# Kernel optimization log

Measured on AMD Instinct MI355X. Metric: run time of the kernel, lower is better.

Reference implementation:

```python
import jax, jax.numpy as jnp
import numpy as np
import math

D_MODEL = 1024
NUM_HEADS = 16
D_KEY = D_MODEL // NUM_HEADS  # 64, used only for the softmax scale
B, S = 4, 2048


def setup_inputs() -> dict:
    key = jax.random.key(0)
    ks = jax.random.split(key, 7)
    scale = 1.0 / math.sqrt(D_MODEL)
    x = jax.random.normal(ks[0], (B, S, D_MODEL), dtype=jnp.float32)
    # torch.nn.Linear params: weight [out, in], bias [out]
    Wq = jax.random.normal(ks[1], (D_MODEL, D_MODEL), dtype=jnp.float32) * scale
    bq = jax.random.normal(ks[2], (D_MODEL,), dtype=jnp.float32) * scale
    Wk = jax.random.normal(ks[3], (D_MODEL, D_MODEL), dtype=jnp.float32) * scale
    bk = jax.random.normal(ks[4], (D_MODEL,), dtype=jnp.float32) * scale
    Wv = jax.random.normal(ks[5], (D_MODEL, D_MODEL), dtype=jnp.float32) * scale
    bv = jax.random.normal(ks[6], (D_MODEL,), dtype=jnp.float32) * scale
    return {"x": x, "Wq": Wq, "bq": bq, "Wk": Wk, "bk": bk, "Wv": Wv, "bv": bv}


def reference(x, Wq, bq, Wk, bk, Wv, bv):
    # Q, K, V projections (torch Linear: x @ W.T + b)
    Q = jnp.einsum('bsd,ed->bse', x, Wq) + bq  # [B,S,D]
    K = jnp.einsum('bsd,ed->bse', x, Wk) + bk
    V = jnp.einsum('bsd,ed->bse', x, Wv) + bv
    inv_sqrt_dk = 1.0 / math.sqrt(D_KEY)
    # full-width attention (no head split, as in the source forward)
    scores = jnp.einsum('bqd,bkd->bqk', Q, K) * inv_sqrt_dk  # [B,S,S]
    weights = jax.nn.softmax(scores, axis=-1)
    return jnp.einsum('bqk,bkd->bqd', weights, V)  # [B,S,D]
```

## Files before the change

kernel.cpp:

```cpp
#include <hip/hip_runtime.h>
#include <stdint.h>

#define S_LEN 2048
#define DMODEL 1024
#define NBATCH 4
#define MROWS (NBATCH * S_LEN)

typedef __bf16 bf16x8 __attribute__((ext_vector_type(8)));
typedef float f32x4 __attribute__((ext_vector_type(4)));

__device__ __forceinline__ unsigned short f2bf(float f) {
  unsigned int x = __builtin_bit_cast(unsigned int, f);
  x += 0x7FFFu + ((x >> 16) & 1u);
  return (unsigned short)(x >> 16);
}

template <int N>
__device__ __forceinline__ void waitvm() {
  static_assert(N <= 8, "vmcnt range");
  if constexpr (N < 0) {}
  else if constexpr (N == 0) asm volatile("s_waitcnt vmcnt(0)" ::: "memory");
  else if constexpr (N == 1) asm volatile("s_waitcnt vmcnt(1)" ::: "memory");
  else if constexpr (N == 2) asm volatile("s_waitcnt vmcnt(2)" ::: "memory");
  else if constexpr (N == 3) asm volatile("s_waitcnt vmcnt(3)" ::: "memory");
  else if constexpr (N == 4) asm volatile("s_waitcnt vmcnt(4)" ::: "memory");
  else if constexpr (N == 5) asm volatile("s_waitcnt vmcnt(5)" ::: "memory");
  else if constexpr (N == 6) asm volatile("s_waitcnt vmcnt(6)" ::: "memory");
  else if constexpr (N == 7) asm volatile("s_waitcnt vmcnt(7)" ::: "memory");
  else asm volatile("s_waitcnt vmcnt(8)" ::: "memory");
}
#define BARRIER() do { __builtin_amdgcn_s_barrier(); asm volatile("" ::: "memory"); } while (0)

__global__ void cvt_kernel(const float* __restrict__ src, ushort4* __restrict__ dst, int n4) {
  int i = blockIdx.x * blockDim.x + threadIdx.x;
  if (i < n4) {
    float4 v = reinterpret_cast<const float4*>(src)[i];
    ushort4 o;
    o.x = f2bf(v.x); o.y = f2bf(v.y); o.z = f2bf(v.z); o.w = f2bf(v.w);
    dst[i] = o;
  }
}

template <int BM_, int EP>
__global__ __launch_bounds__(512, 2) void gemm8(
    const unsigned short* __restrict__ A, const unsigned short* __restrict__ Bm,
    void* __restrict__ Cp, const float* __restrict__ bias,
    int lda, int ldb, int ldc, int NT, float scale,
    long zsA, long zsB, long zsC) {
  constexpr int BN_ = 256;
  constexpr int BK = 64;
  constexpr int RA = BM_ / 128;
  constexpr int HALF_A = (BM_ / 2) * 128;
  constexpr int HALF_B = 128 * 128;
  constexpr int ATILE = BM_ * 128;
  constexpr int BTILE = BN_ * 128;
  constexpr int MREP = BM_ / 32;
  constexpr int MQ = MREP / 2;
  constexpr int VPRO = (BM_ == 256) ? 4 : 3;
  constexpr int V_P0 = (BM_ == 256) ? 4 : 2;
  constexpr int V_P3 = (BM_ == 256) ? 8 : 6;
  constexpr int V_P5 = (BM_ == 256) ? 4 : 3;
  constexpr int VD_P0 = (BM_ == 256) ? 2 : 1;

  __shared__ alignas(16) char lds[(ATILE + BTILE) * 2];

  const int tid = threadIdx.x;
  const int l = tid & 63;
  const int w = tid >> 6;
  const int wm = w >> 2;
  const int wn = w & 3;

  const int gx = gridDim.x;
  const int nwg = gridDim.x * gridDim.y;
  int n = blockIdx.y * gx + blockIdx.x;
  int n2 = (n & 7) * (nwg >> 3) + (n >> 3);
  const int tileM = (n2 / gx) * BM_;
  const int tileN = (n2 % gx) * BN_;

  const int z = blockIdx.z;
  const unsigned short* Ab = A + (size_t)z * zsA;
  const unsigned short* Bb = Bm + (size_t)z * zsB;

  const int srow = l >> 3;
  const int scol = (((l & 7) ^ srow) * 16);

  auto stageA = [&](int buf, int t, int h) {
#pragma unroll
    for (int r = 0; r < RA; ++r) {
      int row = h * (BM_ / 2) + r * 64 + w * 8 + srow;
      const char* g = (const char*)(Ab + (size_t)(tileM + row) * lda + t * BK) + scol;
      char* d = lds + buf * (ATILE + BTILE) + h * HALF_A + r * 8192 + w * 1024;
      __builtin_amdgcn_global_load_lds(
          (const __attribute__((address_space(1))) void*)g,
          (__attribute__((address_space(3))) void*)d, 16, 0, 0);
    }
  };
  auto stageB = [&](int buf, int t, int h) {
#pragma unroll
    for (int r = 0; r < 2; ++r) {
      int row = h * 128 + r * 64 + w * 8 + srow;
      const char* g = (const char*)(Bb + (size_t)(tileN + row) * ldb + t * BK) + scol;
      char* d = lds + buf * (ATILE + BTILE) + ATILE + h * HALF_B + r * 8192 + w * 1024;
      __builtin_amdgcn_global_load_lds(
          (const __attribute__((address_space(1))) void*)g,
          (__attribute__((address_space(3))) void*)d, 16, 0, 0);
    }
  };

  f32x4 acc[MREP][4];
#pragma unroll
  for (int m = 0; m < MREP; ++m)
#pragma unroll
    for (int nn = 0; nn < 4; ++nn) acc[m][nn] = f32x4{0.f, 0.f, 0.f, 0.f};

  const int frow = l & 15;
  auto rdA = [&](int buf, int mh, int m, int kk) -> bf16x8 {
    int row = mh * (BM_ / 2) + wm * (BM_ / 4) + m * 16 + frow;
    int col = (kk * 64 + ((l >> 4) * 16)) ^ ((row & 7) << 4);
    return *reinterpret_cast<const bf16x8*>(lds + buf * (ATILE + BTILE) + row * 128 + col);
  };
  auto rdB = [&](int buf, int nh, int nn, int kk) -> bf16x8 {
    int row = nh * 128 + wn * 32 + nn * 16 + frow;
    int col = (kk * 64 + ((l >> 4) * 16)) ^ ((row & 7) << 4);
    return *reinterpret_cast<const bf16x8*>(lds + buf * (ATILE + BTILE) + ATILE + row * 128 + col);
  };

  bf16x8 avA[MQ], avB[MQ];
  bf16x8 bvv[2][2][2];

  auto rdAset = [&](int buf, int mh, int kk, bf16x8 (&dst)[MQ]) {
#pragma unroll
    for (int m = 0; m < MQ; ++m) dst[m] = rdA(buf, mh, m, kk);
  };
  auto rdBset = [&](int buf, int nh, int kk) {
#pragma unroll
    for (int nn = 0; nn < 2; ++nn) bvv[nh][kk][nn] = rdB(buf, nh, nn, kk);
  };
  auto mf8 = [&](bf16x8 (&av)[MQ], int mh, int nh, int kk) {
    __builtin_amdgcn_s_setprio(1);
#pragma unroll
    for (int m = 0; m < MQ; ++m)
#pragma unroll
      for (int nn = 0; nn < 2; ++nn)
        acc[mh * MQ + m][nh * 2 + nn] = __builtin_amdgcn_mfma_f32_16x16x32_bf16(
            av[m], bvv[nh][kk][nn], acc[mh * MQ + m][nh * 2 + nn], 0, 0, 0);
    __builtin_amdgcn_s_setprio(0);
  };

  stageA(0, 0, 0);
  stageB(0, 0, 0);
  stageB(0, 0, 1);
  stageA(0, 0, 1);
  waitvm<VPRO>();
  BARRIER();

  for (int t = 0; t < NT - 1; ++t) {
    const int buf = t & 1, nb = buf ^ 1;
    rdAset(buf, 0, 0, avA); rdBset(buf, 0, 0);
    stageA(nb, t + 1, 0); waitvm<V_P0>(); BARRIER();
    mf8(avA, 0, 0, 0);
    rdBset(buf, 1, 0);
    stageB(nb, t + 1, 0); BARRIER();
    mf8(avA, 0, 1, 0);
    rdAset(buf, 0, 1, avB); rdBset(buf, 1, 1);
    stageB(nb, t + 1, 1); BARRIER();
    mf8(avB, 0, 1, 1);
    rdBset(buf, 0, 1);
    stageA(nb, t + 1, 1); waitvm<V_P3>(); BARRIER();
    mf8(avB, 0, 0, 1);
    rdAset(buf, 1, 1, avA);
    BARRIER();
    mf8(avA, 1, 0, 1); mf8(avA, 1, 1, 1);
    rdAset(buf, 1, 0, avB);
    waitvm<V_P5>(); BARRIER();
    mf8(avB, 1, 1, 0); mf8(avB, 1, 0, 0);
  }
  {
    const int buf = (NT - 1) & 1;
    rdAset(buf, 0, 0, avA); rdBset(buf, 0, 0); waitvm<VD_P0>(); BARRIER();
    mf8(avA, 0, 0, 0);
    rdBset(buf, 1, 0); BARRIER();
    mf8(avA, 0, 1, 0);
    rdAset(buf, 0, 1, avB); rdBset(buf, 1, 1); BARRIER();
    mf8(avB, 0, 1, 1);
    rdBset(buf, 0, 1); waitvm<0>(); BARRIER();
    mf8(avB, 0, 0, 1);
    rdAset(buf, 1, 1, avA); BARRIER();
    mf8(avA, 1, 0, 1); mf8(avA, 1, 1, 1);
    rdAset(buf, 1, 0, avB); BARRIER();
    mf8(avB, 1, 1, 0); mf8(avB, 1, 0, 0);
  }

  const int lr = (l >> 4) * 4;
  const int lc = l & 15;
#pragma unroll
  for (int mh = 0; mh < 2; ++mh) {
#pragma unroll
    for (int m = 0; m < MQ; ++m) {
#pragma unroll
      for (int nh = 0; nh < 2; ++nh) {
#pragma unroll
        for (int nn = 0; nn < 2; ++nn) {
          int gr = tileM + mh * (BM_ / 2) + wm * (BM_ / 4) + m * 16 + lr;
          int gc = tileN + nh * 128 + wn * 32 + nn * 16 + lc;
          f32x4 v = acc[mh * MQ + m][nh * 2 + nn];
          if constexpr (EP == 0 || EP == 3) {
            unsigned short* C = (unsigned short*)Cp + (size_t)z * zsC;
#pragma unroll
            for (int j = 0; j < 4; ++j) {
              float bb = (EP == 0) ? bias[gc] : bias[gr + j];
              C[(size_t)(gr + j) * ldc + gc] = f2bf(v[j] + bb);
            }
          } else {
            float* C = (float*)Cp + (size_t)z * zsC;
#pragma unroll
            for (int j = 0; j < 4; ++j)
              C[(size_t)(gr + j) * ldc + gc] = (EP == 1) ? v[j] * scale : v[j];
          }
        }
      }
    }
  }
}

__global__ __launch_bounds__(256) void softmax_kernel(const float* __restrict__ Sb,
                                                      unsigned short* __restrict__ P) {
  const size_t row = blockIdx.x;
  const float* sp = Sb + row * S_LEN;
  const int t = threadIdx.x;
  const int wid = t >> 6, lane = t & 63;
  float4 v0 = reinterpret_cast<const float4*>(sp)[t * 2];
  float4 v1 = reinterpret_cast<const float4*>(sp)[t * 2 + 1];
  float s[8] = {v0.x, v0.y, v0.z, v0.w, v1.x, v1.y, v1.z, v1.w};
  float mx = s[0];
#pragma unroll
  for (int i = 1; i < 8; ++i) mx = fmaxf(mx, s[i]);
#pragma unroll
  for (int o = 32; o > 0; o >>= 1) mx = fmaxf(mx, __shfl_xor(mx, o));
  __shared__ float redm[4];
  __shared__ float reds[4];
  if (lane == 0) redm[wid] = mx;
  __syncthreads();
  mx = fmaxf(fmaxf(redm[0], redm[1]), fmaxf(redm[2], redm[3]));
  float e[8];
  float sum = 0.f;
#pragma unroll
  for (int i = 0; i < 8; ++i) { e[i] = __expf(s[i] - mx); sum += e[i]; }
#pragma unroll
  for (int o = 32; o > 0; o >>= 1) sum += __shfl_xor(sum, o);
  if (lane == 0) reds[wid] = sum;
  __syncthreads();
  sum = reds[0] + reds[1] + reds[2] + reds[3];
  float inv = 1.0f / sum;
  ushort4 o0, o1;
  o0.x = f2bf(e[0] * inv); o0.y = f2bf(e[1] * inv); o0.z = f2bf(e[2] * inv); o0.w = f2bf(e[3] * inv);
  o1.x = f2bf(e[4] * inv); o1.y = f2bf(e[5] * inv); o1.z = f2bf(e[6] * inv); o1.w = f2bf(e[7] * inv);
  ushort4* dp = reinterpret_cast<ushort4*>(P + row * S_LEN);
  dp[t * 2] = o0;
  dp[t * 2 + 1] = o1;
}

extern "C" void kernel_launch(void* const* d_in, const int* in_sizes, int n_in,
                              void* d_out, int out_size, void* d_ws, size_t ws_size,
                              hipStream_t stream) {
  (void)in_sizes; (void)n_in; (void)out_size;
  const float* x = (const float*)d_in[0];
  const float* Wq = (const float*)d_in[1];
  const float* bq = (const float*)d_in[2];
  const float* Wk = (const float*)d_in[3];
  const float* bk = (const float*)d_in[4];
  const float* Wv = (const float*)d_in[5];
  const float* bv = (const float*)d_in[6];
  float* out = (float*)d_out;

  if (ws_size < 141557760ull) return;
  char* ws = (char*)d_ws;
  unsigned short* xb   = (unsigned short*)(ws);
  unsigned short* Wqkb = (unsigned short*)(ws + 16777216);
  unsigned short* Wvb  = (unsigned short*)(ws + 20971520);
  float*          bqk  = (float*)(ws + 23068672);
  unsigned short* QKb  = (unsigned short*)(ws + 24117248);
  float*          Sb   = (float*)(ws + 57671680);
  unsigned short* Vt   = (unsigned short*)(ws + 124780544);
  unsigned short* P    = QKb;

  cvt_kernel<<<dim3(MROWS * DMODEL / 4 / 256), 256, 0, stream>>>(x, (ushort4*)xb, MROWS * DMODEL / 4);
  cvt_kernel<<<dim3(1024), 256, 0, stream>>>(Wq, (ushort4*)Wqkb, DMODEL * DMODEL / 4);
  cvt_kernel<<<dim3(1024), 256, 0, stream>>>(Wk, (ushort4*)(Wqkb + 1048576), DMODEL * DMODEL / 4);
  cvt_kernel<<<dim3(1024), 256, 0, stream>>>(Wv, (ushort4*)Wvb, DMODEL * DMODEL / 4);
  hipMemcpyAsync(bqk, bq, 4096, hipMemcpyDeviceToDevice, stream);
  hipMemcpyAsync(bqk + 1024, bk, 4096, hipMemcpyDeviceToDevice, stream);

  gemm8<256, 0><<<dim3(8, 32, 1), 512, 0, stream>>>(
      xb, Wqkb, QKb, bqk, 1024, 1024, 2048, 16, 1.f, 0, 0, 0);

  gemm8<128, 3><<<dim3(8, 8, 4), 512, 0, stream>>>(
      Wvb, xb, Vt, bv, 1024, 1024, 2048, 16, 1.f,
      0, (long)S_LEN * DMODEL, (long)DMODEL * S_LEN);

  gemm8<256, 1><<<dim3(8, 8, 4), 512, 0, stream>>>(
      QKb, QKb + 1024, Sb, nullptr, 2048, 2048, 2048, 16, 0.125f,
      (long)S_LEN * 2048, (long)S_LEN * 2048, (long)S_LEN * S_LEN);

  softmax_kernel<<<dim3(MROWS), 256, 0, stream>>>(Sb, P);

  gemm8<128, 2><<<dim3(4, 16, 4), 512, 0, stream>>>(
      P, Vt, out, nullptr, 2048, 2048, 1024, 32, 1.f,
      (long)S_LEN * S_LEN, (long)DMODEL * S_LEN, (long)S_LEN * DMODEL);
}
```

Before: 176.5 us.

## Fuse weight conversions, make K-loop count compile-time, add explicit LDS waits

Replaces three weight-conversion kernels and two bias memcpys with a single prep kernel, cutting launch count. Makes the GEMM K-tile count a template parameter and unrolls the main loop by two so buffer indices and loop control become constant. Inserts explicit lgkmcnt(0) waits plus scheduling barriers after each block barrier. These pin the instruction order around the MFMA phases but may serialize LDS reads against compute the compiler could otherwise overlap.

```diff
diff --git a/kernel.cpp b/kernel.cpp
--- a/kernel.cpp
+++ b/kernel.cpp
@@ -30,6 +30,8 @@
   else asm volatile("s_waitcnt vmcnt(8)" ::: "memory");
 }
 #define BARRIER() do { __builtin_amdgcn_s_barrier(); asm volatile("" ::: "memory"); } while (0)
+#define LGKM0() do { asm volatile("s_waitcnt lgkmcnt(0)" ::: "memory"); \
+                     __builtin_amdgcn_sched_barrier(0); } while (0)
 
 __global__ void cvt_kernel(const float* __restrict__ src, ushort4* __restrict__ dst, int n4) {
   int i = blockIdx.x * blockDim.x + threadIdx.x;
@@ -41,11 +43,29 @@
   }
 }
 
-template <int BM_, int EP>
+__global__ void prep_kernel(const float* __restrict__ Wq, const float* __restrict__ Wk,
+                            const float* __restrict__ Wv, const float* __restrict__ bq,
+                            const float* __restrict__ bk, ushort4* __restrict__ Wqkb,
+                            ushort4* __restrict__ Wvb, float4* __restrict__ bqk) {
+  const int NW = DMODEL * DMODEL / 4;
+  int i = blockIdx.x * blockDim.x + threadIdx.x;
+  float4 v;
+  if (i < NW) v = reinterpret_cast<const float4*>(Wq)[i];
+  else if (i < 2 * NW) v = reinterpret_cast<const float4*>(Wk)[i - NW];
+  else v = reinterpret_cast<const float4*>(Wv)[i - 2 * NW];
+  ushort4 o;
+  o.x = f2bf(v.x); o.y = f2bf(v.y); o.z = f2bf(v.z); o.w = f2bf(v.w);
+  if (i < 2 * NW) Wqkb[i] = o;
+  else Wvb[i - 2 * NW] = o;
+  if (i < 512) bqk[i] = (i < 256) ? reinterpret_cast<const float4*>(bq)[i]
+                                  : reinterpret_cast<const float4*>(bk)[i - 256];
+}
+
+template <int BM_, int EP, int NT>
 __global__ __launch_bounds__(512, 2) void gemm8(
     const unsigned short* __restrict__ A, const unsigned short* __restrict__ Bm,
     void* __restrict__ Cp, const float* __restrict__ bias,
-    int lda, int ldb, int ldc, int NT, float scale,
+    int lda, int ldb, int ldc, float scale,
     long zsA, long zsB, long zsC) {
   constexpr int BN_ = 256;
   constexpr int BK = 64;
@@ -154,40 +174,41 @@
   waitvm<VPRO>();
   BARRIER();
 
+#pragma unroll 2
   for (int t = 0; t < NT - 1; ++t) {
     const int buf = t & 1, nb = buf ^ 1;
     rdAset(buf, 0, 0, avA); rdBset(buf, 0, 0);
-    stageA(nb, t + 1, 0); waitvm<V_P0>(); BARRIER();
+    stageA(nb, t + 1, 0); waitvm<V_P0>(); BARRIER(); LGKM0();
     mf8(avA, 0, 0, 0);
     rdBset(buf, 1, 0);
-    stageB(nb, t + 1, 0); BARRIER();
+    stageB(nb, t + 1, 0); BARRIER(); LGKM0();
     mf8(avA, 0, 1, 0);
     rdAset(buf, 0, 1, avB); rdBset(buf, 1, 1);
-    stageB(nb, t + 1, 1); BARRIER();
+    stageB(nb, t + 1, 1); BARRIER(); LGKM0();
     mf8(avB, 0, 1, 1);
     rdBset(buf, 0, 1);
-    stageA(nb, t + 1, 1); waitvm<V_P3>(); BARRIER();
+    stageA(nb, t + 1, 1); waitvm<V_P3>(); BARRIER(); LGKM0();
     mf8(avB, 0, 0, 1);
     rdAset(buf, 1, 1, avA);
-    BARRIER();
+    BARRIER(); LGKM0();
     mf8(avA, 1, 0, 1); mf8(avA, 1, 1, 1);
     rdAset(buf, 1, 0, avB);
-    waitvm<V_P5>(); BARRIER();
+    waitvm<V_P5>(); BARRIER(); LGKM0();
     mf8(avB, 1, 1, 0); mf8(avB, 1, 0, 0);
   }
   {
     const int buf = (NT - 1) & 1;
-    rdAset(buf, 0, 0, avA); rdBset(buf, 0, 0); waitvm<VD_P0>(); BARRIER();
+    rdAset(buf, 0, 0, avA); rdBset(buf, 0, 0); waitvm<VD_P0>(); BARRIER(); LGKM0();
     mf8(avA, 0, 0, 0);
-    rdBset(buf, 1, 0); BARRIER();
+    rdBset(buf, 1, 0); BARRIER(); LGKM0();
     mf8(avA, 0, 1, 0);
-    rdAset(buf, 0, 1, avB); rdBset(buf, 1, 1); BARRIER();
+    rdAset(buf, 0, 1, avB); rdBset(buf, 1, 1); BARRIER(); LGKM0();
     mf8(avB, 0, 1, 1);
-    rdBset(buf, 0, 1); waitvm<0>(); BARRIER();
+    rdBset(buf, 0, 1); waitvm<0>(); BARRIER(); LGKM0();
     mf8(avB, 0, 0, 1);
-    rdAset(buf, 1, 1, avA); BARRIER();
+    rdAset(buf, 1, 1, avA); BARRIER(); LGKM0();
     mf8(avA, 1, 0, 1); mf8(avA, 1, 1, 1);
-    rdAset(buf, 1, 0, avB); BARRIER();
+    rdAset(buf, 1, 0, avB); BARRIER(); LGKM0();
     mf8(avB, 1, 1, 0); mf8(avB, 1, 0, 0);
   }
 
@@ -285,26 +306,23 @@
   unsigned short* P    = QKb;
 
   cvt_kernel<<<dim3(MROWS * DMODEL / 4 / 256), 256, 0, stream>>>(x, (ushort4*)xb, MROWS * DMODEL / 4);
-  cvt_kernel<<<dim3(1024), 256, 0, stream>>>(Wq, (ushort4*)Wqkb, DMODEL * DMODEL / 4);
-  cvt_kernel<<<dim3(1024), 256, 0, stream>>>(Wk, (ushort4*)(Wqkb + 1048576), DMODEL * DMODEL / 4);
-  cvt_kernel<<<dim3(1024), 256, 0, stream>>>(Wv, (ushort4*)Wvb, DMODEL * DMODEL / 4);
-  hipMemcpyAsync(bqk, bq, 4096, hipMemcpyDeviceToDevice, stream);
-  hipMemcpyAsync(bqk + 1024, bk, 4096, hipMemcpyDeviceToDevice, stream);
-
-  gemm8<256, 0><<<dim3(8, 32, 1), 512, 0, stream>>>(
-      xb, Wqkb, QKb, bqk, 1024, 1024, 2048, 16, 1.f, 0, 0, 0);
-
-  gemm8<128, 3><<<dim3(8, 8, 4), 512, 0, stream>>>(
-      Wvb, xb, Vt, bv, 1024, 1024, 2048, 16, 1.f,
+  prep_kernel<<<dim3(3 * DMODEL * DMODEL / 4 / 256), 256, 0, stream>>>(
+      Wq, Wk, Wv, bq, bk, (ushort4*)Wqkb, (ushort4*)Wvb, (float4*)bqk);
+
+  gemm8<256, 0, 16><<<dim3(8, 32, 1), 512, 0, stream>>>(
+      xb, Wqkb, QKb, bqk, 1024, 1024, 2048, 1.f, 0, 0, 0);
+
+  gemm8<128, 3, 16><<<dim3(8, 8, 4), 512, 0, stream>>>(
+      Wvb, xb, Vt, bv, 1024, 1024, 2048, 1.f,
       0, (long)S_LEN * DMODEL, (long)DMODEL * S_LEN);
 
-  gemm8<256, 1><<<dim3(8, 8, 4), 512, 0, stream>>>(
-      QKb, QKb + 1024, Sb, nullptr, 2048, 2048, 2048, 16, 0.125f,
+  gemm8<256, 1, 16><<<dim3(8, 8, 4), 512, 0, stream>>>(
+      QKb, QKb + 1024, Sb, nullptr, 2048, 2048, 2048, 0.125f,
       (long)S_LEN * 2048, (long)S_LEN * 2048, (long)S_LEN * S_LEN);
 
   softmax_kernel<<<dim3(MROWS), 256, 0, stream>>>(Sb, P);
 
-  gemm8<128, 2><<<dim3(4, 16, 4), 512, 0, stream>>>(
-      P, Vt, out, nullptr, 2048, 2048, 1024, 32, 1.f,
+  gemm8<128, 2, 32><<<dim3(4, 16, 4), 512, 0, stream>>>(
+      P, Vt, out, nullptr, 2048, 2048, 1024, 1.f,
       (long)S_LEN * S_LEN, (long)DMODEL * S_LEN, (long)S_LEN * DMODEL);
 }
```

Result: faster. 167.7 us (-5.0%).
